# Kernel tuning notes

Measured on AMD Instinct MI355X. Metric: run time of the kernel, lower is better.

The kernel has to match this reference:

```python
import jax, jax.numpy as jnp
import numpy as np

N_EMBD = 1024
N_HEAD = 16
HEAD = N_EMBD // N_HEAD  # 64
N_HIDDEN = 2816          # ((int(2*4*1024/3)-1)//256)*256 + 256
BLOCK_SIZE = 4096
EPS = 1e-5


def rope_cos_sin(T, hd, base=10000.0):
    theta = 1.0 / (base ** (jnp.arange(0, hd, 2, dtype=jnp.float32) / hd))  # (hd/2,)
    idx = jnp.arange(T, dtype=jnp.float32)
    ang = jnp.outer(idx, theta)  # (T, hd/2)
    return jnp.cos(ang), jnp.sin(ang)


def apply_rope(x, cos, sin):
    # x: (B, H, T, hd); rotate interleaved pairs (x0,x1),(x2,x3),...
    xp = x.reshape(*x.shape[:-1], HEAD // 2, 2)
    xe, xo = xp[..., 0], xp[..., 1]
    c = cos[None, None, :, :]
    s = sin[None, None, :, :]
    oe = xe * c - xo * s
    oo = xe * s + xo * c
    return jnp.stack([oe, oo], axis=-1).reshape(x.shape)


def rmsnorm(x, scale):
    ms = jnp.mean(x * x, axis=-1, keepdims=True)
    return scale * (x * jax.lax.rsqrt(ms + EPS))


def setup_inputs() -> dict:
    key = jax.random.key(0)
    ks = jax.random.split(key, 9)
    B, T = 2, 2048
    x = jax.random.normal(ks[0], (B, T, N_EMBD), dtype=jnp.float32)
    y_mask = jax.random.randint(ks[1], (B, 64), 0, 2, dtype=jnp.int32)
    sd = 1.0 / np.sqrt(N_EMBD)
    Wqkv = jax.random.normal(ks[2], (N_EMBD, 3 * N_EMBD), dtype=jnp.float32) * sd
    Wattn_proj = jax.random.normal(ks[3], (N_EMBD, N_EMBD), dtype=jnp.float32) * sd
    scale1 = jnp.ones((N_EMBD,), dtype=jnp.float32)
    scale2 = jnp.ones((N_EMBD,), dtype=jnp.float32)
    Wfc1 = jax.random.normal(ks[4], (N_EMBD, N_HIDDEN), dtype=jnp.float32) * sd
    Wfc2 = jax.random.normal(ks[5], (N_EMBD, N_HIDDEN), dtype=jnp.float32) * sd
    Wmlp_proj = jax.random.normal(ks[6], (N_HIDDEN, N_EMBD), dtype=jnp.float32) / np.sqrt(N_HIDDEN)
    return {"x": x, "y_mask": y_mask, "Wqkv": Wqkv, "Wattn_proj": Wattn_proj,
            "scale1": scale1, "scale2": scale2, "Wfc1": Wfc1, "Wfc2": Wfc2,
            "Wmlp_proj": Wmlp_proj}


def reference(x, y_mask, Wqkv, Wattn_proj, scale1, scale2, Wfc1, Wfc2, Wmlp_proj):
    B, T, C = x.shape
    # ---- attention branch (pre-RMSNorm) ----
    h = rmsnorm(x, scale1)
    qkv = h @ Wqkv  # (B, T, 3C)
    q, k, v = jnp.split(qkv, 3, axis=-1)
    q = q.reshape(B, T, N_HEAD, HEAD).transpose(0, 2, 1, 3)
    k = k.reshape(B, T, N_HEAD, HEAD).transpose(0, 2, 1, 3)
    v = v.reshape(B, T, N_HEAD, HEAD).transpose(0, 2, 1, 3)
    cos, sin = rope_cos_sin(T, HEAD)
    q = apply_rope(q, cos, sin)
    k = apply_rope(k, cos, sin)
    # mixed causal + text-text bidirectional mask
    causal = jnp.tril(jnp.ones((T, T), dtype=bool))  # (T, T)
    ym = y_mask.astype(bool)  # (B, L)
    L = ym.shape[1]
    text = ym[:, :, None] & ym[:, None, :]  # (B, L, L)
    text = jnp.pad(text, ((0, 0), (0, T - L), (0, T - L)))
    mask = jnp.logical_or(causal[None, :, :], text)  # (B, T, T)
    scale = 1.0 / np.sqrt(HEAD)
    scores = jnp.einsum('bhqd,bhkd->bhqk', q, k) * scale
    scores = jnp.where(mask[:, None, :, :], scores, -jnp.inf)
    attn = jax.nn.softmax(scores, axis=-1)
    y = jnp.einsum('bhqk,bhkd->bhqd', attn, v)
    y = y.transpose(0, 2, 1, 3).reshape(B, T, C)
    x = x + y @ Wattn_proj
    # ---- SwiGLU MLP branch (pre-RMSNorm) ----
    h2 = rmsnorm(x, scale2)
    m = jax.nn.silu(h2 @ Wfc1) * (h2 @ Wfc2)
    x = x + m @ Wmlp_proj
    return x
```

## Files before the change

### kernel.cpp

```cpp
#include <hip/hip_runtime.h>
#include <stdint.h>

typedef unsigned short u16;
typedef __attribute__((ext_vector_type(8))) short bf16x8;
typedef __attribute__((ext_vector_type(4))) float f32x4;

__device__ __forceinline__ float b2f(u16 u) {
    union { float f; uint32_t u; } v; v.u = ((uint32_t)u) << 16; return v.f;
}
__device__ __forceinline__ u16 f2b(float f) {
    union { float f; uint32_t u; } v; v.f = f;
    uint32_t r = v.u + 0x7FFFu + ((v.u >> 16) & 1u);
    return (u16)(r >> 16);
}
__device__ __forceinline__ uint32_t cvt_pk_bf16(float lo, float hi) {
    uint32_t r;
    asm("v_cvt_pk_bf16_f32 %0, %1, %2" : "=v"(r) : "v"(lo), "v"(hi));
    return r;
}

template <int CTRL>
__device__ __forceinline__ float dppf(float x) {
    union { float f; int i; } u; u.f = x;
    u.i = __builtin_amdgcn_update_dpp(0, u.i, CTRL, 0xF, 0xF, false);
    return u.f;
}
__device__ __forceinline__ float rowmax16(float v) {
    v = fmaxf(v, dppf<0x121>(v));
    v = fmaxf(v, dppf<0x122>(v));
    v = fmaxf(v, dppf<0x124>(v));
    v = fmaxf(v, dppf<0x128>(v));
    return v;
}
__device__ __forceinline__ float rowsum16(float v) {
    v += dppf<0x121>(v);
    v += dppf<0x122>(v);
    v += dppf<0x124>(v);
    v += dppf<0x128>(v);
    return v;
}

__device__ __forceinline__ void stage16(const void* g, void* l) {
    __builtin_amdgcn_global_load_lds(
        (const __attribute__((address_space(1))) uint32_t*)(uintptr_t)g,
        (__attribute__((address_space(3))) uint32_t*)(uint32_t)(uintptr_t)l,
        16, 0, 0);
}

__global__ __launch_bounds__(256) void prep_kernel(const float* __restrict__ Wqkv,
                                                   const float* __restrict__ Wattn,
                                                   const float* __restrict__ Wfc1,
                                                   const float* __restrict__ Wfc2,
                                                   const float* __restrict__ Wmlp,
                                                   u16* WtQ, u16* WtA, u16* WtF1,
                                                   u16* WtF2, u16* WtM,
                                                   const float* __restrict__ xin,
                                                   const float* __restrict__ scale,
                                                   u16* __restrict__ xout) {
    const int tx = threadIdx.x, ty = threadIdx.y;
    int id = blockIdx.x;
    if (id >= 12544) {
        const int row = id - 12544, tid = ty * 32 + tx;
        const float4 v = ((const float4*)(xin + (size_t)row * 1024))[tid];
        float ss = v.x * v.x + v.y * v.y + v.z * v.z + v.w * v.w;
        #pragma unroll
        for (int d = 32; d; d >>= 1) ss += __shfl_xor(ss, d);
        __shared__ float wsum[4];
        if ((tid & 63) == 0) wsum[tid >> 6] = ss;
        __syncthreads();
        const float r = rsqrtf((wsum[0] + wsum[1] + wsum[2] + wsum[3]) * (1.f / 1024.f) + 1e-5f);
        const float4 sc = ((const float4*)scale)[tid];
        uint2 o;
        o.x = cvt_pk_bf16(v.x * sc.x * r, v.y * sc.y * r);
        o.y = cvt_pk_bf16(v.z * sc.z * r, v.w * sc.w * r);
        ((uint2*)(xout + (size_t)row * 1024))[tid] = o;
        return;
    }
    __shared__ u16 tile[32][33];
    const float* src; u16* dst; int R, C;
    if (id < 3072)      {             src = Wqkv;  dst = WtQ;  R = 1024; C = 3072; }
    else if (id < 4096) { id -= 3072; src = Wattn; dst = WtA;  R = 1024; C = 1024; }
    else if (id < 6912) { id -= 4096; src = Wfc1;  dst = WtF1; R = 1024; C = 2816; }
    else if (id < 9728) { id -= 6912; src = Wfc2;  dst = WtF2; R = 1024; C = 2816; }
    else                { id -= 9728; src = Wmlp;  dst = WtM;  R = 2816; C = 1024; }
    const int nbx = C >> 5;
    const int bx = id % nbx, by = id / nbx;
    const int cx = bx * 32, ry = by * 32;
    #pragma unroll
    for (int i = 0; i < 32; i += 8)
        tile[ty + i][tx] = f2b(src[(size_t)(ry + ty + i) * C + cx + tx]);
    __syncthreads();
    #pragma unroll
    for (int i = 0; i < 32; i += 8)
        dst[(size_t)(cx + ty + i) * R + ry + tx] = tile[tx][ty + i];
}

__global__ __launch_bounds__(256) void rmsnorm_f32(const float* __restrict__ xin,
                                                   const float* __restrict__ scale,
                                                   u16* __restrict__ out) {
    const int row = blockIdx.x, tid = threadIdx.x;
    const float4 v = ((const float4*)(xin + (size_t)row * 1024))[tid];
    float ss = v.x * v.x + v.y * v.y + v.z * v.z + v.w * v.w;
    #pragma unroll
    for (int d = 32; d; d >>= 1) ss += __shfl_xor(ss, d);
    __shared__ float wsum[4];
    if ((tid & 63) == 0) wsum[tid >> 6] = ss;
    __syncthreads();
    const float r = rsqrtf((wsum[0] + wsum[1] + wsum[2] + wsum[3]) * (1.f / 1024.f) + 1e-5f);
    const float4 sc = ((const float4*)scale)[tid];
    uint2 o;
    o.x = cvt_pk_bf16(v.x * sc.x * r, v.y * sc.y * r);
    o.y = cvt_pk_bf16(v.z * sc.z * r, v.w * sc.w * r);
    ((uint2*)(out + (size_t)row * 1024))[tid] = o;
}

__global__ __launch_bounds__(256) void rope_kernel(u16* __restrict__ qkv) {
    const int gid = blockIdx.x * 256 + threadIdx.x;
    const int i = gid & 31;
    const int row = gid >> 5;
    const int tpos = row & 2047;
    const float theta = expf(-(float)i * (9.210340371976184f / 32.0f));
    const float ang = (float)tpos * theta;
    const float c = cosf(ang), s = sinf(ang);
    uint32_t* p = (uint32_t*)qkv + (size_t)row * 1536 + i;
    #pragma unroll
    for (int h = 0; h < 16; ++h) {
        const uint32_t uq = p[h * 32];
        {
            const float xe = b2f((u16)(uq & 0xffff)), xo = b2f((u16)(uq >> 16));
            p[h * 32] = cvt_pk_bf16(xe * c - xo * s, xe * s + xo * c);
        }
        const uint32_t uk = p[512 + h * 32];
        {
            const float xe = b2f((u16)(uk & 0xffff)), xo = b2f((u16)(uk >> 16));
            p[512 + h * 32] = cvt_pk_bf16(xe * c - xo * s, xe * s + xo * c);
        }
    }
}

template <int EPI>
__global__ __launch_bounds__(256) void gemm_bt(const u16* __restrict__ A,
                                               const u16* __restrict__ Bt,
                                               void* __restrict__ Cout,
                                               const void* __restrict__ Res,
                                               int N, int K) {
    __shared__ __attribute__((aligned(16))) u16 As[2][128 * 32];
    __shared__ __attribute__((aligned(16))) u16 Bs[2][128 * 32];
    const int tid = threadIdx.x;
    const int w = tid >> 6, lane = tid & 63;
    const int quad = lane >> 4, t = lane & 15;
    const int m0 = blockIdx.y * 128, n0 = blockIdx.x * 128;
    const int wm = (w >> 1) * 64, wn = (w & 1) * 64;

    const int srow = w * 16 + (lane >> 2);
    const int scol = (lane & 3) * 8;
    const u16* pA0 = A + (size_t)(m0 + srow) * K + scol;
    const u16* pA1 = pA0 + (size_t)64 * K;
    const u16* pB0 = Bt + (size_t)(n0 + srow) * K + scol;
    const u16* pB1 = pB0 + (size_t)64 * K;

    f32x4 acc[4][4];
    #pragma unroll
    for (int i = 0; i < 4; ++i)
        #pragma unroll
        for (int j = 0; j < 4; ++j) acc[i][j] = (f32x4){0.f, 0.f, 0.f, 0.f};

    for (int kb = 0; kb < K; kb += 64) {
        __syncthreads();
        stage16(pA0 + kb,      (char*)As[0] + w * 1024);
        stage16(pA1 + kb,      (char*)As[0] + 4096 + w * 1024);
        stage16(pB0 + kb,      (char*)Bs[0] + w * 1024);
        stage16(pB1 + kb,      (char*)Bs[0] + 4096 + w * 1024);
        stage16(pA0 + kb + 32, (char*)As[1] + w * 1024);
        stage16(pA1 + kb + 32, (char*)As[1] + 4096 + w * 1024);
        stage16(pB0 + kb + 32, (char*)Bs[1] + w * 1024);
        stage16(pB1 + kb + 32, (char*)Bs[1] + 4096 + w * 1024);
        __syncthreads();
        #pragma unroll
        for (int hf = 0; hf < 2; ++hf) {
            bf16x8 af[4], bfr[4];
            #pragma unroll
            for (int mi = 0; mi < 4; ++mi)
                af[mi] = *(const bf16x8*)((char*)As[hf] + (wm + mi * 16 + t) * 64 + quad * 16);
            #pragma unroll
            for (int ni = 0; ni < 4; ++ni)
                bfr[ni] = *(const bf16x8*)((char*)Bs[hf] + (wn + ni * 16 + t) * 64 + quad * 16);
            #pragma unroll
            for (int mi = 0; mi < 4; ++mi)
                #pragma unroll
                for (int ni = 0; ni < 4; ++ni)
                    acc[mi][ni] = __builtin_amdgcn_mfma_f32_16x16x32_bf16(af[mi], bfr[ni],
                                                                         acc[mi][ni], 0, 0, 0);
        }
    }
    #pragma unroll
    for (int mi = 0; mi < 4; ++mi) {
        const int row0 = m0 + wm + mi * 16 + quad * 4;
        #pragma unroll
        for (int ni = 0; ni < 4; ++ni) {
            const int col = n0 + wn + ni * 16 + t;
            #pragma unroll
            for (int r = 0; r < 4; r += 2) {
                const size_t idx0 = (size_t)(row0 + r) * N + col;
                const size_t idx1 = (size_t)(row0 + r + 1) * N + col;
                if (EPI == 0) {
                    const uint32_t pk2 = cvt_pk_bf16(acc[mi][ni][r], acc[mi][ni][r + 1]);
                    ((u16*)Cout)[idx0] = (u16)pk2;
                    ((u16*)Cout)[idx1] = (u16)(pk2 >> 16);
                } else {
                    ((float*)Cout)[idx0] = acc[mi][ni][r]     + ((const float*)Res)[idx0];
                    ((float*)Cout)[idx1] = acc[mi][ni][r + 1] + ((const float*)Res)[idx1];
                }
            }
        }
    }
}

template <int EPI>
__global__ __launch_bounds__(256) void gemm_bt64(const u16* __restrict__ A,
                                                 const u16* __restrict__ Bt,
                                                 void* __restrict__ Cout,
                                                 const float* __restrict__ Res,
                                                 int N, int K) {
    __shared__ __attribute__((aligned(16))) u16 As[2][128 * 32];
    __shared__ __attribute__((aligned(16))) u16 Bs[2][64 * 32];
    const int tid = threadIdx.x;
    const int w = tid >> 6, lane = tid & 63;
    const int quad = lane >> 4, t = lane & 15;
    const int m0 = blockIdx.y * 128, n0 = blockIdx.x * 64;
    const int wm = (w >> 1) * 64, wn = (w & 1) * 32;

    const int srow = w * 16 + (lane >> 2);
    const int scol = (lane & 3) * 8;
    const u16* pA0 = A + (size_t)(m0 + srow) * K + scol;
    const u16* pA1 = pA0 + (size_t)64 * K;
    const u16* pB0 = Bt + (size_t)(n0 + srow) * K + scol;

    f32x4 acc[4][2];
    #pragma unroll
    for (int i = 0; i < 4; ++i)
        #pragma unroll
        for (int j = 0; j < 2; ++j) acc[i][j] = (f32x4){0.f, 0.f, 0.f, 0.f};

    for (int kb = 0; kb < K; kb += 64) {
        __syncthreads();
        stage16(pA0 + kb,      (char*)As[0] + w * 1024);
        stage16(pA1 + kb,      (char*)As[0] + 4096 + w * 1024);
        stage16(pB0 + kb,      (char*)Bs[0] + w * 1024);
        stage16(pA0 + kb + 32, (char*)As[1] + w * 1024);
        stage16(pA1 + kb + 32, (char*)As[1] + 4096 + w * 1024);
        stage16(pB0 + kb + 32, (char*)Bs[1] + w * 1024);
        __syncthreads();
        #pragma unroll
        for (int hf = 0; hf < 2; ++hf) {
            bf16x8 af[4], bfr[2];
            #pragma unroll
            for (int mi = 0; mi < 4; ++mi)
                af[mi] = *(const bf16x8*)((char*)As[hf] + (wm + mi * 16 + t) * 64 + quad * 16);
            #pragma unroll
            for (int ni = 0; ni < 2; ++ni)
                bfr[ni] = *(const bf16x8*)((char*)Bs[hf] + (wn + ni * 16 + t) * 64 + quad * 16);
            #pragma unroll
            for (int mi = 0; mi < 4; ++mi)
                #pragma unroll
                for (int ni = 0; ni < 2; ++ni)
                    acc[mi][ni] = __builtin_amdgcn_mfma_f32_16x16x32_bf16(af[mi], bfr[ni],
                                                                         acc[mi][ni], 0, 0, 0);
        }
    }
    #pragma unroll
    for (int mi = 0; mi < 4; ++mi) {
        const int row0 = m0 + wm + mi * 16 + quad * 4;
        #pragma unroll
        for (int ni = 0; ni < 2; ++ni) {
            const int col = n0 + wn + ni * 16 + t;
            #pragma unroll
            for (int r = 0; r < 4; ++r) {
                const size_t idx = (size_t)(row0 + r) * N + col;
                const float v = acc[mi][ni][r];
                if (EPI == 0) ((u16*)Cout)[idx]   = f2b(v);
                else          ((float*)Cout)[idx] = v + Res[idx];
            }
        }
    }
}

__global__ __launch_bounds__(256) void gemm_fc(const u16* __restrict__ A,
                                               const u16* __restrict__ B1t,
                                               const u16* __restrict__ B2t,
                                               u16* __restrict__ Cout,
                                               int N, int K) {
    __shared__ __attribute__((aligned(16))) u16 As[2][128 * 32];
    __shared__ __attribute__((aligned(16))) u16 B1s[2][64 * 32];
    __shared__ __attribute__((aligned(16))) u16 B2s[2][64 * 32];
    const int tid = threadIdx.x;
    const int w = tid >> 6, lane = tid & 63;
    const int quad = lane >> 4, t = lane & 15;
    const int m0 = blockIdx.y * 128, n0 = blockIdx.x * 64;
    const int wm = (w >> 1) * 64, wn = (w & 1) * 32;

    const int srow = w * 16 + (lane >> 2);
    const int scol = (lane & 3) * 8;
    const u16* pA0 = A + (size_t)(m0 + srow) * K + scol;
    const u16* pA1 = pA0 + (size_t)64 * K;
    const u16* pB1 = B1t + (size_t)(n0 + srow) * K + scol;
    const u16* pB2 = B2t + (size_t)(n0 + srow) * K + scol;

    f32x4 acc1[4][2], acc2[4][2];
    #pragma unroll
    for (int i = 0; i < 4; ++i)
        #pragma unroll
        for (int j = 0; j < 2; ++j) {
            acc1[i][j] = (f32x4){0.f, 0.f, 0.f, 0.f};
            acc2[i][j] = (f32x4){0.f, 0.f, 0.f, 0.f};
        }

    for (int kb = 0; kb < K; kb += 64) {
        __syncthreads();
        stage16(pA0 + kb,      (char*)As[0] + w * 1024);
        stage16(pA1 + kb,      (char*)As[0] + 4096 + w * 1024);
        stage16(pB1 + kb,      (char*)B1s[0] + w * 1024);
        stage16(pB2 + kb,      (char*)B2s[0] + w * 1024);
        stage16(pA0 + kb + 32, (char*)As[1] + w * 1024);
        stage16(pA1 + kb + 32, (char*)As[1] + 4096 + w * 1024);
        stage16(pB1 + kb + 32, (char*)B1s[1] + w * 1024);
        stage16(pB2 + kb + 32, (char*)B2s[1] + w * 1024);
        __syncthreads();
        #pragma unroll
        for (int hf = 0; hf < 2; ++hf) {
            bf16x8 af[4], b1r[2], b2r[2];
            #pragma unroll
            for (int mi = 0; mi < 4; ++mi)
                af[mi] = *(const bf16x8*)((char*)As[hf] + (wm + mi * 16 + t) * 64 + quad * 16);
            #pragma unroll
            for (int ni = 0; ni < 2; ++ni) {
                b1r[ni] = *(const bf16x8*)((char*)B1s[hf] + (wn + ni * 16 + t) * 64 + quad * 16);
                b2r[ni] = *(const bf16x8*)((char*)B2s[hf] + (wn + ni * 16 + t) * 64 + quad * 16);
            }
            #pragma unroll
            for (int mi = 0; mi < 4; ++mi)
                #pragma unroll
                for (int ni = 0; ni < 2; ++ni) {
                    acc1[mi][ni] = __builtin_amdgcn_mfma_f32_16x16x32_bf16(af[mi], b1r[ni],
                                                                          acc1[mi][ni], 0, 0, 0);
                    acc2[mi][ni] = __builtin_amdgcn_mfma_f32_16x16x32_bf16(af[mi], b2r[ni],
                                                                          acc2[mi][ni], 0, 0, 0);
                }
        }
    }
    #pragma unroll
    for (int mi = 0; mi < 4; ++mi) {
        const int row0 = m0 + wm + mi * 16 + quad * 4;
        #pragma unroll
        for (int ni = 0; ni < 2; ++ni) {
            const int col = n0 + wn + ni * 16 + t;
            float mv[4];
            #pragma unroll
            for (int r = 0; r < 4; ++r) {
                const float a = acc1[mi][ni][r];
                mv[r] = (a / (1.f + __expf(-a))) * acc2[mi][ni][r];
            }
            #pragma unroll
            for (int r = 0; r < 4; r += 2) {
                const uint32_t pk2 = cvt_pk_bf16(mv[r], mv[r + 1]);
                Cout[(size_t)(row0 + r) * N + col]     = (u16)pk2;
                Cout[(size_t)(row0 + r + 1) * N + col] = (u16)(pk2 >> 16);
            }
        }
    }
}

__global__ __launch_bounds__(256) void attn_kernel(const u16* __restrict__ qkv,
                                                   const int* __restrict__ ymask,
                                                   u16* __restrict__ y) {
    const int gid = blockIdx.x;
    const int xcd = gid & 7;
    const int j2 = gid >> 3;
    const int slot = j2 >> 4;
    const int pairk = j2 & 15;
    const int group = slot * 8 + xcd;
    const int h = group & 15, b = group >> 4;
    const int tid = threadIdx.x;
    const int w = tid >> 6, lane = tid & 63;
    const int quad = lane >> 4, t = lane & 15;

    __shared__ __attribute__((aligned(16))) u16 Ks[64 * 72];
    __shared__ __attribute__((aligned(16))) u16 Vts[64 * 72];
    __shared__ __attribute__((aligned(16))) u16 Ps[4][16 * 72];
    __shared__ int ymL[64];
    if (pairk == 0 && tid < 64) ymL[tid] = ymask[b * 64 + tid];

    const int skey = tid >> 3, sdg = tid & 7;
    const u16* pK = qkv + (size_t)(b * 2048 + skey) * 3072 + h * 64 + sdg * 8 + 1024;
    const int sblk0 = (skey >> 3) ^ sdg;
    const int sblk1 = (4 + (skey >> 3)) ^ sdg;

    for (int seg = 0; seg < 2; ++seg) {
        const int qt = seg ? pairk : 31 - pairk;
        const int q0 = qt * 64;

        bf16x8 aQ[2];
        {
            const u16* qp = qkv + (size_t)(b * 2048 + q0 + w * 16 + t) * 3072 + h * 64 + quad * 8;
            aQ[0] = *(const bf16x8*)qp;
            aQ[1] = *(const bf16x8*)(qp + 32);
            #pragma unroll
            for (int i = 0; i < 8; ++i) {
                aQ[0][i] = (short)f2b(b2f((u16)aQ[0][i]) * 0.125f);
                aQ[1][i] = (short)f2b(b2f((u16)aQ[1][i]) * 0.125f);
            }
        }

        f32x4 accO[4] = {(f32x4){0,0,0,0},(f32x4){0,0,0,0},(f32x4){0,0,0,0},(f32x4){0,0,0,0}};
        float mOld[4] = {-INFINITY, -INFINITY, -INFINITY, -INFINITY};
        float lSum[4] = {0.f, 0.f, 0.f, 0.f};

        for (int kb = 0; kb <= qt; ++kb) {
            const u16* pk = pK + (size_t)kb * 196608;
            const uint4 kv0 = *(const uint4*)pk;
            const uint4 vv0 = *(const uint4*)(pk + 1024);
            const uint4 kv1 = *(const uint4*)(pk + 98304);
            const uint4 vv1 = *(const uint4*)(pk + 99328);
            __syncthreads();
            *(uint4*)((char*)Ks + skey * 144 + sdg * 16) = kv0;
            *(uint4*)((char*)Ks + (skey + 32) * 144 + sdg * 16) = kv1;
            {
                const u16* vp0 = (const u16*)&vv0;
                const u16* vp1 = (const u16*)&vv1;
                #pragma unroll
                for (int jj = 0; jj < 8; ++jj) {
                    const int row = sdg * 8 + jj;
                    Vts[row * 72 + sblk0 * 8 + (skey & 7)] = vp0[jj];
                    Vts[row * 72 + sblk1 * 8 + (skey & 7)] = vp1[jj];
                }
            }
            __syncthreads();

            float s[4][4];
            __builtin_amdgcn_s_setprio(1);
            #pragma unroll
            for (int ni = 0; ni < 4; ++ni) {
                bf16x8 bK0 = *(const bf16x8*)((char*)Ks + (ni * 16 + t) * 144 + quad * 16);
                bf16x8 bK1 = *(const bf16x8*)((char*)Ks + (ni * 16 + t) * 144 + 64 + quad * 16);
                f32x4 sa = (f32x4){0.f, 0.f, 0.f, 0.f};
                sa = __builtin_amdgcn_mfma_f32_16x16x32_bf16(aQ[0], bK0, sa, 0, 0, 0);
                sa = __builtin_amdgcn_mfma_f32_16x16x32_bf16(aQ[1], bK1, sa, 0, 0, 0);
                #pragma unroll
                for (int r = 0; r < 4; ++r) s[ni][r] = sa[r];
            }
            __builtin_amdgcn_s_setprio(0);

            if (kb == qt) {
                const int irow = q0 + w * 16 + quad * 4;
                #pragma unroll
                for (int ni = 0; ni < 4; ++ni)
                    #pragma unroll
                    for (int r = 0; r < 4; ++r) {
                        const int i = irow + r, j = kb * 64 + ni * 16 + t;
                        const bool ok = (j <= i) || (qt == 0 && ymL[i & 63] && ymL[j & 63]);
                        if (!ok) s[ni][r] = -INFINITY;
                    }
            }

            float alpha[4];
            bool upd = false;
            #pragma unroll
            for (int r = 0; r < 4; ++r) {
                float mt = fmaxf(fmaxf(s[0][r], s[1][r]), fmaxf(s[2][r], s[3][r]));
                mt = rowmax16(mt);
                const float mNew = fmaxf(mOld[r], mt);
                upd = upd || (mNew > mOld[r]);
                alpha[r] = __expf(mOld[r] - mNew);
                #pragma unroll
                for (int ni = 0; ni < 4; ++ni) s[ni][r] = __expf(s[ni][r] - mNew);
                mOld[r] = mNew;
            }

            u16* Pw = Ps[w];
            #pragma unroll
            for (int ni = 0; ni < 4; ++ni)
                #pragma unroll
                for (int r = 0; r < 4; r += 2) {
                    const uint32_t pk2 = cvt_pk_bf16(s[ni][r], s[ni][r + 1]);
                    Pw[(quad * 4 + r) * 72 + ni * 16 + t]     = (u16)pk2;
                    Pw[(quad * 4 + r + 1) * 72 + ni * 16 + t] = (u16)(pk2 >> 16);
                }

            #pragma unroll
            for (int r = 0; r < 4; ++r) {
                float rs = (s[0][r] + s[1][r]) + (s[2][r] + s[3][r]);
                rs = rowsum16(rs);
                lSum[r] = lSum[r] * alpha[r] + rs;
            }
            if (__any(upd)) {
                #pragma unroll
                for (int dt = 0; dt < 4; ++dt)
                    #pragma unroll
                    for (int r = 0; r < 4; ++r) accO[dt][r] *= alpha[r];
            }

            bf16x8 aP0 = *(const bf16x8*)((char*)Pw + t * 144 + quad * 16);
            bf16x8 aP1 = *(const bf16x8*)((char*)Pw + t * 144 + 64 + quad * 16);
            __builtin_amdgcn_s_setprio(1);
            #pragma unroll
            for (int dt = 0; dt < 4; ++dt) {
                const int row = dt * 16 + t, rb = row >> 3;
                bf16x8 bV0 = *(const bf16x8*)((char*)Vts + row * 144 + ((quad ^ rb) << 4));
                bf16x8 bV1 = *(const bf16x8*)((char*)Vts + row * 144 + (((4 + quad) ^ rb) << 4));
                accO[dt] = __builtin_amdgcn_mfma_f32_16x16x32_bf16(aP0, bV0, accO[dt], 0, 0, 0);
                accO[dt] = __builtin_amdgcn_mfma_f32_16x16x32_bf16(aP1, bV1, accO[dt], 0, 0, 0);
            }
            __builtin_amdgcn_s_setprio(0);
        }
        const int orow = q0 + w * 16 + quad * 4;
        float ri[4];
        #pragma unroll
        for (int r = 0; r < 4; ++r) ri[r] = __builtin_amdgcn_rcpf(lSum[r]);
        #pragma unroll
        for (int dt = 0; dt < 4; ++dt)
            #pragma unroll
            for (int r = 0; r < 4; r += 2) {
                const uint32_t pk2 = cvt_pk_bf16(accO[dt][r] * ri[r], accO[dt][r + 1] * ri[r + 1]);
                y[(size_t)(b * 2048 + orow + r) * 1024 + h * 64 + dt * 16 + t]     = (u16)pk2;
                y[(size_t)(b * 2048 + orow + r + 1) * 1024 + h * 64 + dt * 16 + t] = (u16)(pk2 >> 16);
            }
    }
}

extern "C" void kernel_launch(void* const* d_in, const int* in_sizes, int n_in,
                              void* d_out, int out_size, void* d_ws, size_t ws_size,
                              hipStream_t stream) {
    const float* x     = (const float*)d_in[0];
    const int*   ym    = (const int*)d_in[1];
    const float* Wqkv  = (const float*)d_in[2];
    const float* Wattn = (const float*)d_in[3];
    const float* s1    = (const float*)d_in[4];
    const float* s2    = (const float*)d_in[5];
    const float* Wfc1  = (const float*)d_in[6];
    const float* Wfc2  = (const float*)d_in[7];
    const float* Wmlp  = (const float*)d_in[8];

    char* ws = (char*)d_ws;
    u16*   h    = (u16*)(ws + 0);
    u16*   qkv  = (u16*)(ws + 8388608);
    u16*   fc1  = qkv;
    float* xr   = (float*)(ws + 33554432);
    u16*   WtA  = (u16*)(ws + 50331648);
    u16*   WtF1 = (u16*)(ws + 52428800);
    u16*   WtF2 = (u16*)(ws + 58195968);
    u16*   WtM  = (u16*)(ws + 63963136);
    u16*   WtQ  = (u16*)(ws + 73400320);
    const dim3 tb(32, 8);

    prep_kernel<<<16640, tb, 0, stream>>>(Wqkv, Wattn, Wfc1, Wfc2, Wmlp,
                                          WtQ, WtA, WtF1, WtF2, WtM, x, s1, h);
    gemm_bt<0><<<dim3(24, 32), 256, 0, stream>>>(h, WtQ, qkv, nullptr, 3072, 1024);
    rope_kernel<<<512, 256, 0, stream>>>(qkv);
    attn_kernel<<<512, 256, 0, stream>>>(qkv, ym, h);
    gemm_bt64<1><<<dim3(16, 32), 256, 0, stream>>>(h, WtA, xr, x, 1024, 1024);
    rmsnorm_f32<<<4096, 256, 0, stream>>>(xr, s2, h);
    gemm_fc<<<dim3(44, 32), 256, 0, stream>>>(h, WtF1, WtF2, fc1, 2816, 1024);
    gemm_bt64<1><<<dim3(16, 32), 256, 0, stream>>>(fc1, WtM, (float*)d_out, xr, 1024, 2816);
}
```

Before: 354.3 us.

## Fuse RoPE into QKV GEMM epilogue with precomputed cos/sin table

Removes the separate rope_kernel launch and applies the rotary embedding in the QKV GEMM epilogue for the q and k column blocks, using a DPP lane swap to fetch the pair partner. A cos/sin table is now computed by extra blocks in the prep kernel and stored in workspace. Packed bf16 conversions in the epilogues and attention stores are replaced with scalar f2b stores, and the rcp is replaced with a true division. This saves one pass over qkv in global memory, at the cost of a heavier epilogue with table loads and more scalar stores.

```diff
diff --git a/kernel.cpp b/kernel.cpp
--- a/kernel.cpp
+++ b/kernel.cpp
@@ -56,9 +56,18 @@
                                                    u16* WtF2, u16* WtM,
                                                    const float* __restrict__ xin,
                                                    const float* __restrict__ scale,
-                                                   u16* __restrict__ xout) {
+                                                   u16* __restrict__ xout,
+                                                   float2* __restrict__ ctab) {
     const int tx = threadIdx.x, ty = threadIdx.y;
     int id = blockIdx.x;
+    if (id >= 16640) {
+        const int e = (id - 16640) * 256 + ty * 32 + tx;
+        const int tpos = e >> 5, j = e & 31;
+        const float theta = expf(-(float)j * (9.210340371976184f / 32.0f));
+        const float ang = (float)tpos * theta;
+        ctab[e] = make_float2(cosf(ang), sinf(ang));
+        return;
+    }
     if (id >= 12544) {
         const int row = id - 12544, tid = ty * 32 + tx;
         const float4 v = ((const float4*)(xin + (size_t)row * 1024))[tid];
@@ -114,36 +123,11 @@
     ((uint2*)(out + (size_t)row * 1024))[tid] = o;
 }
 
-__global__ __launch_bounds__(256) void rope_kernel(u16* __restrict__ qkv) {
-    const int gid = blockIdx.x * 256 + threadIdx.x;
-    const int i = gid & 31;
-    const int row = gid >> 5;
-    const int tpos = row & 2047;
-    const float theta = expf(-(float)i * (9.210340371976184f / 32.0f));
-    const float ang = (float)tpos * theta;
-    const float c = cosf(ang), s = sinf(ang);
-    uint32_t* p = (uint32_t*)qkv + (size_t)row * 1536 + i;
-    #pragma unroll
-    for (int h = 0; h < 16; ++h) {
-        const uint32_t uq = p[h * 32];
-        {
-            const float xe = b2f((u16)(uq & 0xffff)), xo = b2f((u16)(uq >> 16));
-            p[h * 32] = cvt_pk_bf16(xe * c - xo * s, xe * s + xo * c);
-        }
-        const uint32_t uk = p[512 + h * 32];
-        {
-            const float xe = b2f((u16)(uk & 0xffff)), xo = b2f((u16)(uk >> 16));
-            p[512 + h * 32] = cvt_pk_bf16(xe * c - xo * s, xe * s + xo * c);
-        }
-    }
-}
-
-template <int EPI>
-__global__ __launch_bounds__(256) void gemm_bt(const u16* __restrict__ A,
-                                               const u16* __restrict__ Bt,
-                                               void* __restrict__ Cout,
-                                               const void* __restrict__ Res,
-                                               int N, int K) {
+__global__ __launch_bounds__(256) void gemm_qkv(const u16* __restrict__ A,
+                                                const u16* __restrict__ Bt,
+                                                u16* __restrict__ Cout,
+                                                const float2* __restrict__ ctab,
+                                                int N, int K) {
     __shared__ __attribute__((aligned(16))) u16 As[2][128 * 32];
     __shared__ __attribute__((aligned(16))) u16 Bs[2][128 * 32];
     const int tid = threadIdx.x;
@@ -193,24 +177,35 @@
                                                                          acc[mi][ni], 0, 0, 0);
         }
     }
-    #pragma unroll
-    for (int mi = 0; mi < 4; ++mi) {
-        const int row0 = m0 + wm + mi * 16 + quad * 4;
-        #pragma unroll
-        for (int ni = 0; ni < 4; ++ni) {
-            const int col = n0 + wn + ni * 16 + t;
-            #pragma unroll
-            for (int r = 0; r < 4; r += 2) {
-                const size_t idx0 = (size_t)(row0 + r) * N + col;
-                const size_t idx1 = (size_t)(row0 + r + 1) * N + col;
-                if (EPI == 0) {
-                    const uint32_t pk2 = cvt_pk_bf16(acc[mi][ni][r], acc[mi][ni][r + 1]);
-                    ((u16*)Cout)[idx0] = (u16)pk2;
-                    ((u16*)Cout)[idx1] = (u16)(pk2 >> 16);
-                } else {
-                    ((float*)Cout)[idx0] = acc[mi][ni][r]     + ((const float*)Res)[idx0];
-                    ((float*)Cout)[idx1] = acc[mi][ni][r + 1] + ((const float*)Res)[idx1];
+    if (blockIdx.x < 16) {
+        const float sgn = (t & 1) ? 1.f : -1.f;
+        #pragma unroll
+        for (int mi = 0; mi < 4; ++mi) {
+            const int row0 = m0 + wm + mi * 16 + quad * 4;
+            #pragma unroll
+            for (int ni = 0; ni < 4; ++ni) {
+                const int col = n0 + wn + ni * 16 + t;
+                const int j = (ni * 16 + t) >> 1;
+                #pragma unroll
+                for (int r = 0; r < 4; ++r) {
+                    const int row = row0 + r;
+                    const float2 cs = ctab[(size_t)(row & 2047) * 32 + j];
+                    const float own = acc[mi][ni][r];
+                    const float par = dppf<0xB1>(own);
+                    Cout[(size_t)row * N + col] = f2b(own * cs.x + par * (sgn * cs.y));
                 }
+            }
+        }
+    } else {
+        #pragma unroll
+        for (int mi = 0; mi < 4; ++mi) {
+            const int row0 = m0 + wm + mi * 16 + quad * 4;
+            #pragma unroll
+            for (int ni = 0; ni < 4; ++ni) {
+                const int col = n0 + wn + ni * 16 + t;
+                #pragma unroll
+                for (int r = 0; r < 4; ++r)
+                    Cout[(size_t)(row0 + r) * N + col] = f2b(acc[mi][ni][r]);
             }
         }
     }
@@ -480,11 +475,8 @@
             #pragma unroll
             for (int ni = 0; ni < 4; ++ni)
                 #pragma unroll
-                for (int r = 0; r < 4; r += 2) {
-                    const uint32_t pk2 = cvt_pk_bf16(s[ni][r], s[ni][r + 1]);
-                    Pw[(quad * 4 + r) * 72 + ni * 16 + t]     = (u16)pk2;
-                    Pw[(quad * 4 + r + 1) * 72 + ni * 16 + t] = (u16)(pk2 >> 16);
-                }
+                for (int r = 0; r < 4; ++r)
+                    Pw[(quad * 4 + r) * 72 + ni * 16 + t] = f2b(s[ni][r]);
 
             #pragma unroll
             for (int r = 0; r < 4; ++r) {
@@ -513,16 +505,12 @@
             __builtin_amdgcn_s_setprio(0);
         }
         const int orow = q0 + w * 16 + quad * 4;
-        float ri[4];
-        #pragma unroll
-        for (int r = 0; r < 4; ++r) ri[r] = __builtin_amdgcn_rcpf(lSum[r]);
         #pragma unroll
         for (int dt = 0; dt < 4; ++dt)
             #pragma unroll
-            for (int r = 0; r < 4; r += 2) {
-                const uint32_t pk2 = cvt_pk_bf16(accO[dt][r] * ri[r], accO[dt][r + 1] * ri[r + 1]);
-                y[(size_t)(b * 2048 + orow + r) * 1024 + h * 64 + dt * 16 + t]     = (u16)pk2;
-                y[(size_t)(b * 2048 + orow + r + 1) * 1024 + h * 64 + dt * 16 + t] = (u16)(pk2 >> 16);
+            for (int r = 0; r < 4; ++r) {
+                const size_t idx = (size_t)(b * 2048 + orow + r) * 1024 + h * 64 + dt * 16 + t;
+                y[idx] = f2b(accO[dt][r] / lSum[r]);
             }
     }
 }
@@ -541,21 +529,21 @@
     const float* Wmlp  = (const float*)d_in[8];
 
     char* ws = (char*)d_ws;
-    u16*   h    = (u16*)(ws + 0);
-    u16*   qkv  = (u16*)(ws + 8388608);
-    u16*   fc1  = qkv;
-    float* xr   = (float*)(ws + 33554432);
-    u16*   WtA  = (u16*)(ws + 50331648);
-    u16*   WtF1 = (u16*)(ws + 52428800);
-    u16*   WtF2 = (u16*)(ws + 58195968);
-    u16*   WtM  = (u16*)(ws + 63963136);
-    u16*   WtQ  = (u16*)(ws + 73400320);
+    u16*    h    = (u16*)(ws + 0);
+    u16*    qkv  = (u16*)(ws + 8388608);
+    u16*    fc1  = qkv;
+    float*  xr   = (float*)(ws + 33554432);
+    u16*    WtA  = (u16*)(ws + 50331648);
+    u16*    WtF1 = (u16*)(ws + 52428800);
+    u16*    WtF2 = (u16*)(ws + 58195968);
+    u16*    WtM  = (u16*)(ws + 63963136);
+    float2* ctab = (float2*)(ws + 69730304);
+    u16*    WtQ  = (u16*)(ws + 73400320);
     const dim3 tb(32, 8);
 
-    prep_kernel<<<16640, tb, 0, stream>>>(Wqkv, Wattn, Wfc1, Wfc2, Wmlp,
-                                          WtQ, WtA, WtF1, WtF2, WtM, x, s1, h);
-    gemm_bt<0><<<dim3(24, 32), 256, 0, stream>>>(h, WtQ, qkv, nullptr, 3072, 1024);
-    rope_kernel<<<512, 256, 0, stream>>>(qkv);
+    prep_kernel<<<16896, tb, 0, stream>>>(Wqkv, Wattn, Wfc1, Wfc2, Wmlp,
+                                          WtQ, WtA, WtF1, WtF2, WtM, x, s1, h, ctab);
+    gemm_qkv<<<dim3(24, 32), 256, 0, stream>>>(h, WtQ, qkv, ctab, 3072, 1024);
     attn_kernel<<<512, 256, 0, stream>>>(qkv, ym, h);
     gemm_bt64<1><<<dim3(16, 32), 256, 0, stream>>>(h, WtA, xr, x, 1024, 1024);
     rmsnorm_f32<<<4096, 256, 0, stream>>>(xr, s2, h);
```

After: 369.9 us. 1.04x slower.
